# Kernel optimization log

Hardware: AMD Instinct MI355X
Metric: run time of the kernel (lower is better)

Reference implementation:

```python
import jax, jax.numpy as jnp
import numpy as np

N = 50000
E = 800000
IN_C = 128
HID = 64
HEADS = 4
NUM_CLASSES = 10
NUM_GRAPHS = 64
EPS = 1e-5
NEG_SLOPE = 0.2


def setup_inputs() -> dict:
    key = jax.random.key(0)
    ks = jax.random.split(key, 32)
    inp = {}
    inp["x"] = jax.random.normal(ks[0], (N, IN_C), dtype=jnp.float32)
    inp["edge_index"] = jax.random.randint(ks[1], (2, E), 0, N, dtype=jnp.int32)
    inp["batch"] = jnp.sort(jax.random.randint(ks[2], (N,), 0, NUM_GRAPHS, dtype=jnp.int32))
    s = 0.05
    # GATConv1: in=128 -> heads=4, hid=64, concat -> 256
    inp["W1"] = jax.random.normal(ks[3], (IN_C, HEADS * HID), dtype=jnp.float32) * s
    inp["a_src1"] = jax.random.normal(ks[4], (HEADS, HID), dtype=jnp.float32) * s
    inp["a_dst1"] = jax.random.normal(ks[5], (HEADS, HID), dtype=jnp.float32) * s
    inp["b1"] = jnp.zeros((HEADS * HID,), dtype=jnp.float32)
    inp["g1"] = jnp.ones((HEADS * HID,), dtype=jnp.float32)
    inp["be1"] = jnp.zeros((HEADS * HID,), dtype=jnp.float32)
    # GATConv2: in=256 -> heads=4, hid=64, concat -> 256
    inp["W2"] = jax.random.normal(ks[6], (HEADS * HID, HEADS * HID), dtype=jnp.float32) * s
    inp["a_src2"] = jax.random.normal(ks[7], (HEADS, HID), dtype=jnp.float32) * s
    inp["a_dst2"] = jax.random.normal(ks[8], (HEADS, HID), dtype=jnp.float32) * s
    inp["b2"] = jnp.zeros((HEADS * HID,), dtype=jnp.float32)
    inp["g2"] = jnp.ones((HEADS * HID,), dtype=jnp.float32)
    inp["be2"] = jnp.zeros((HEADS * HID,), dtype=jnp.float32)
    # GATConv3: in=256 -> heads=1, hid=64, mean (concat=False) -> 64
    inp["W3"] = jax.random.normal(ks[9], (HEADS * HID, 1 * HID), dtype=jnp.float32) * s
    inp["a_src3"] = jax.random.normal(ks[10], (1, HID), dtype=jnp.float32) * s
    inp["a_dst3"] = jax.random.normal(ks[11], (1, HID), dtype=jnp.float32) * s
    inp["b3"] = jnp.zeros((HID,), dtype=jnp.float32)
    inp["g3"] = jnp.ones((HID,), dtype=jnp.float32)
    inp["be3"] = jnp.zeros((HID,), dtype=jnp.float32)
    # final classifier
    inp["fcW"] = jax.random.normal(ks[12], (HID, NUM_CLASSES), dtype=jnp.float32) * s
    inp["fcb"] = jnp.zeros((NUM_CLASSES,), dtype=jnp.float32)
    return inp


def gat_conv(x, src, dst, W, a_src, a_dst, b, heads, out_c, concat):
    # Linear transform, split heads: [N, H, C]
    h = (x @ W).reshape(-1, heads, out_c)
    # Per-node attention logits (dot with per-head attention vectors): [N, H]
    as_ = jnp.einsum("nhc,hc->nh", h, a_src)
    ad_ = jnp.einsum("nhc,hc->nh", h, a_dst)
    # Per-edge unnormalized attention (src contributes a_src, dst a_dst)
    e = jax.nn.leaky_relu(as_[src] + ad_[dst], NEG_SLOPE)  # [E, H]
    # Segment softmax over destination node (stable)
    e_max = jax.ops.segment_max(e, dst, num_segments=N)  # [N, H]
    ex = jnp.exp(e - e_max[dst])
    denom = jax.ops.segment_sum(ex, dst, num_segments=N)  # [N, H]
    alpha = ex / denom[dst]  # [E, H]
    # Weighted scatter-aggregate of source features
    msg = h[src] * alpha[:, :, None]  # [E, H, C]
    out = jax.ops.segment_sum(msg, dst, num_segments=N)  # [N, H, C]
    out = out.reshape(-1, heads * out_c) if concat else out.mean(axis=1)
    return out + b


def batch_norm(x, gamma, beta):
    mean = x.mean(axis=0)
    var = x.var(axis=0)
    return (x - mean) * jax.lax.rsqrt(var + EPS) * gamma + beta


def reference(x, edge_index, batch, W1, a_src1, a_dst1, b1, g1, be1,
              W2, a_src2, a_dst2, b2, g2, be2,
              W3, a_src3, a_dst3, b3, g3, be3, fcW, fcb):
    src, dst = edge_index[0], edge_index[1]
    h = jax.nn.relu(gat_conv(x, src, dst, W1, a_src1, a_dst1, b1, HEADS, HID, True))
    h = batch_norm(h, g1, be1)  # dropout = identity (eval)
    h = jax.nn.relu(gat_conv(h, src, dst, W2, a_src2, a_dst2, b2, HEADS, HID, True))
    h = batch_norm(h, g2, be2)
    h = jax.nn.relu(gat_conv(h, src, dst, W3, a_src3, a_dst3, b3, 1, HID, False))
    h = batch_norm(h, g3, be3)
    # global mean pool over graphs
    sums = jax.ops.segment_sum(h, batch, num_segments=NUM_GRAPHS)  # [G, HID]
    counts = jax.ops.segment_sum(jnp.ones((h.shape[0],), h.dtype), batch, num_segments=NUM_GRAPHS)
    pooled = sums / jnp.maximum(counts, 1.0)[:, None]
    return pooled @ fcW + fcb
```

## Files before the change

kernel.cpp:

```cpp
#include <hip/hip_runtime.h>
#include <hip/hip_bf16.h>

#define N_NODES 50000
#define NUM_E   800000
#define EPS_BN  1e-5f
#define NUM_GRAPHS 64
#define NCOPY 64

typedef __attribute__((ext_vector_type(8))) short bf16x8;
typedef __attribute__((ext_vector_type(4))) float f32x4;
typedef unsigned short ushort_t;
typedef unsigned int uint_t;

static __device__ __forceinline__ unsigned short f2bf(float f) {
    unsigned int u = __float_as_uint(f);
    u += 0x7fffu + ((u >> 16) & 1u);
    return (unsigned short)(u >> 16);
}
static __device__ __forceinline__ uint_t pkbf(float lo, float hi) {
    __hip_bfloat162 t = __float22bfloat162_rn(make_float2(lo, hi));
    return *(uint_t*)&t;
}
static __device__ __forceinline__ float bflo(uint_t u) { return __uint_as_float(u << 16); }
static __device__ __forceinline__ float bfhi(uint_t u) { return __uint_as_float(u & 0xffff0000u); }

__global__ void hist_prep_kernel(const int* __restrict__ ei, int* __restrict__ deg,
                                 const float* __restrict__ W1, const float* __restrict__ W2,
                                 const float* __restrict__ W3, const float* __restrict__ x,
                                 ushort_t* __restrict__ w1t, ushort_t* __restrict__ w2t,
                                 ushort_t* __restrict__ w3t, ushort_t* __restrict__ xbf) {
    const int HB = (NUM_E + 255) / 256;
    const int S1 = 128 * 256, S2 = 256 * 256, S3 = 256 * 64;
    const int SW = S1 + S2 + S3;
    const int SX = N_NODES * 128 / 4;
    int b = blockIdx.x;
    if (b < HB) {
        int e = b * 256 + threadIdx.x;
        if (e < NUM_E) atomicAdd(&deg[ei[NUM_E + e]], 1);
        return;
    }
    int i = (b - HB) * 256 + threadIdx.x;
    if (i < SX) {
        float4 v = ((const float4*)x)[i];
        ((uint2*)xbf)[i] = make_uint2(pkbf(v.x, v.y), pkbf(v.z, v.w));
    } else if (i < SX + SW) {
        int j = i - SX;
        if (j < S1) {
            int k = j / 256, n = j % 256;
            w1t[n * 128 + k] = f2bf(W1[j]);
        } else if (j < S1 + S2) {
            int jj = j - S1; int k = jj / 256, n = jj % 256;
            w2t[n * 256 + k] = f2bf(W2[jj]);
        } else {
            int jj = j - S1 - S2; int k = jj / 64, n = jj % 64;
            w3t[n * 256 + k] = f2bf(W3[jj]);
        }
    }
}

__global__ void scan_local_kernel(const int* __restrict__ deg, int* __restrict__ rowptr,
                                  int* __restrict__ bsum) {
    __shared__ int ws[4];
    int b = blockIdx.x, t = threadIdx.x;
    int i = b * 256 + t;
    int lane = t & 63, wv = t >> 6;
    int v = (i < N_NODES) ? deg[i] : 0;
    int incl = v;
#pragma unroll
    for (int off = 1; off < 64; off <<= 1) {
        int u = __shfl_up(incl, off, 64);
        if (lane >= off) incl += u;
    }
    if (lane == 63) ws[wv] = incl;
    __syncthreads();
    if (t == 0) {
        int s = 0;
#pragma unroll
        for (int k = 0; k < 4; ++k) { int x = ws[k]; ws[k] = s; s += x; }
        bsum[b] = s;
    }
    __syncthreads();
    if (i < N_NODES) rowptr[i + 1] = ws[wv] + incl;
}

__global__ __launch_bounds__(256) void scan_fixup_kernel(int* __restrict__ rowptr,
                                                         const int* __restrict__ bsum) {
    __shared__ int ws[4];
    int b = blockIdx.x, t = threadIdx.x;
    int lane = t & 63, wv = t >> 6;
    int v = (t < b) ? bsum[t] : 0;
#pragma unroll
    for (int off = 1; off < 64; off <<= 1) v += __shfl_xor(v, off, 64);
    if (lane == 0) ws[wv] = v;
    __syncthreads();
    int pre = ws[0] + ws[1] + ws[2] + ws[3];
    int i = b * 256 + t;
    if (i < N_NODES) rowptr[i + 1] += pre;
    if (b == 0 && t == 0) rowptr[0] = 0;
}

template<int K, int NFULL, int BN, bool SCAT>
__global__ __launch_bounds__(256) void gemm_fused_kernel(const ushort_t* __restrict__ A,
                                                         const ushort_t* __restrict__ Bt,
                                                         ushort_t* __restrict__ C,
                                                         const float* __restrict__ stats,
                                                         const float* __restrict__ g,
                                                         const float* __restrict__ be,
                                                         const float* __restrict__ a_src,
                                                         const float* __restrict__ a_dst,
                                                         float* __restrict__ as_,
                                                         float* __restrict__ ad_,
                                                         const int* __restrict__ ei,
                                                         const int* __restrict__ rowptr,
                                                         int* __restrict__ fill,
                                                         int* __restrict__ srcs) {
    constexpr int GBX = (N_NODES + 127) / 128;
    if constexpr (SCAT) {
        if (blockIdx.x >= GBX) {
            int idx = (blockIdx.x - GBX) + 1563 * blockIdx.y;
            int e = idx * 256 + (int)threadIdx.x;
            if (e < NUM_E) {
                int dst = ei[NUM_E + e];
                int pos = rowptr[dst] + atomicAdd(&fill[dst], 1);
                srcs[pos] = ei[e];
            }
            return;
        }
    }
    const int NT = BN / 16;
    const int NG = BN / 64;
    constexpr int LOOP_BYTES = (128 * 40 + BN * 40) * 2;
    constexpr int EPI_BYTES  = 4 * 32 * 64 * 2;
    constexpr int SMEM_BYTES = LOOP_BYTES > EPI_BYTES ? LOOP_BYTES : EPI_BYTES;
    __shared__ __align__(16) unsigned char smem[SMEM_BYTES];
    ushort_t (*As)[40]     = (ushort_t (*)[40])smem;
    ushort_t (*Bs)[40]     = (ushort_t (*)[40])(smem + 128 * 40 * 2);
    ushort_t (*Cs)[32][64] = (ushort_t (*)[32][64])smem;
    __shared__ __align__(16) float aff_a[K], aff_b[K];
    __shared__ float asrc_s[BN], adst_s[BN];
    int tid = threadIdx.x;
    int lane = tid & 63, w = tid >> 6;
    int row0 = blockIdx.x * 128, col0 = blockIdx.y * BN;
    int m_l = lane & 15, q = lane >> 4;

    for (int c = tid; c < K; c += 256) {
        float a = 1.f, b = 0.f;
        if (stats) {
            float s0 = 0.f, s1 = 0.f;
#pragma unroll 8
            for (int j = 0; j < NCOPY; ++j) {
                s0 += stats[j * 512 + c];
                s1 += stats[j * 512 + 256 + c];
            }
            float m = s0 * (1.f / N_NODES);
            float var = fmaxf(s1 * (1.f / N_NODES) - m * m, 0.f);
            float rs = rsqrtf(var + EPS_BN) * g[c];
            a = rs; b = be[c] - m * rs;
        }
        aff_a[c] = a; aff_b[c] = b;
    }
    if (tid < BN) {
        asrc_s[tid] = a_src[col0 + tid];
        adst_s[tid] = a_dst[col0 + tid];
    }
    __syncthreads();

    f32x4 acc[2][NT];
#pragma unroll
    for (int r = 0; r < 2; ++r)
#pragma unroll
        for (int c = 0; c < NT; ++c) acc[r][c] = (f32x4){0.f, 0.f, 0.f, 0.f};

    int ar = tid >> 1, ako = (tid & 1) * 16;

    for (int k0 = 0; k0 < K; k0 += 32) {
        uint_t ow[8];
        int gr = row0 + ar;
        uint4 u0 = make_uint4(0, 0, 0, 0), u1 = make_uint4(0, 0, 0, 0);
        if (gr < N_NODES) {
            const ushort_t* ap = A + (long)gr * K + k0 + ako;
            u0 = *(const uint4*)ap;
            u1 = *(const uint4*)(ap + 8);
        }
        uint_t uu[8] = {u0.x, u0.y, u0.z, u0.w, u1.x, u1.y, u1.z, u1.w};
#pragma unroll
        for (int t = 0; t < 8; ++t) {
            int k = k0 + ako + t * 2;
            float lo = bflo(uu[t]) * aff_a[k] + aff_b[k];
            float hi = bfhi(uu[t]) * aff_a[k + 1] + aff_b[k + 1];
            ow[t] = pkbf(lo, hi);
        }
        if constexpr (BN == 128) {
            int br = tid >> 1, bko = (tid & 1) * 16;
            const ushort_t* bp = Bt + (long)(col0 + br) * K + k0 + bko;
            uint4 b0 = *(const uint4*)bp;
            uint4 b1 = *(const uint4*)(bp + 8);
            *(uint4*)&As[ar][ako] = make_uint4(ow[0], ow[1], ow[2], ow[3]);
            *(uint4*)&As[ar][ako + 8] = make_uint4(ow[4], ow[5], ow[6], ow[7]);
            *(uint4*)&Bs[br][bko] = b0;
            *(uint4*)&Bs[br][bko + 8] = b1;
        } else {
            int br = tid >> 2, bko = (tid & 3) * 8;
            uint4 bv = *(const uint4*)(Bt + (long)(col0 + br) * K + k0 + bko);
            *(uint4*)&As[ar][ako] = make_uint4(ow[0], ow[1], ow[2], ow[3]);
            *(uint4*)&As[ar][ako + 8] = make_uint4(ow[4], ow[5], ow[6], ow[7]);
            *(uint4*)&Bs[br][bko] = bv;
        }
        __syncthreads();

        bf16x8 af[2];
#pragma unroll
        for (int r = 0; r < 2; ++r)
            af[r] = *(const bf16x8*)&As[w * 32 + r * 16 + m_l][q * 8];
#pragma unroll
        for (int c = 0; c < NT; ++c) {
            bf16x8 bf = *(const bf16x8*)&Bs[c * 16 + m_l][q * 8];
#pragma unroll
            for (int r = 0; r < 2; ++r)
                acc[r][c] = __builtin_amdgcn_mfma_f32_16x16x32_bf16(af[r], bf, acc[r][c], 0, 0, 0);
        }
        __syncthreads();
    }

    const int H = NFULL / 64;
#pragma unroll
    for (int gblk = 0; gblk < NG; ++gblk) {
        int hidx = blockIdx.y * NG + gblk;
        int colg = col0 + gblk * 64;
#pragma unroll
        for (int r = 0; r < 2; ++r)
#pragma unroll
            for (int cc = 0; cc < 4; ++cc)
#pragma unroll
                for (int i = 0; i < 4; ++i)
                    Cs[w][r * 16 + q * 4 + i][cc * 16 + m_l] = f2bf(acc[r][gblk * 4 + cc][i]);
#pragma unroll
        for (int j = 0; j < 4; ++j) {
            int flat = j * 64 + lane;
            int lr = flat >> 3, chg = flat & 7;
            int gr = row0 + w * 32 + lr;
            uint4 u = *(uint4*)&Cs[w][lr][chg * 8];
            float f0 = bflo(u.x), f1 = bfhi(u.x), f2 = bflo(u.y), f3 = bfhi(u.y);
            float f4 = bflo(u.z), f5 = bfhi(u.z), f6 = bflo(u.w), f7 = bfhi(u.w);
            int cb = gblk * 64 + chg * 8;
            float s1 = f0 * asrc_s[cb] + f1 * asrc_s[cb + 1] + f2 * asrc_s[cb + 2] + f3 * asrc_s[cb + 3]
                     + f4 * asrc_s[cb + 4] + f5 * asrc_s[cb + 5] + f6 * asrc_s[cb + 6] + f7 * asrc_s[cb + 7];
            float s2 = f0 * adst_s[cb] + f1 * adst_s[cb + 1] + f2 * adst_s[cb + 2] + f3 * adst_s[cb + 3]
                     + f4 * adst_s[cb + 4] + f5 * adst_s[cb + 5] + f6 * adst_s[cb + 6] + f7 * adst_s[cb + 7];
#pragma unroll
            for (int o = 1; o < 8; o <<= 1) {
                s1 += __shfl_xor(s1, o, 64);
                s2 += __shfl_xor(s2, o, 64);
            }
            if (gr < N_NODES) {
                *(uint4*)(C + (long)gr * NFULL + colg + chg * 8) = u;
                if ((lane & 7) == 0) {
                    as_[gr * H + hidx] = s1;
                    ad_[gr * H + hidx] = s2;
                }
            }
        }
    }
}

__global__ __launch_bounds__(256) void agg4_kernel(const ushort_t* __restrict__ h,
                                                   const float* __restrict__ as_,
                                                   const float* __restrict__ ad_,
                                                   const int* __restrict__ rowptr,
                                                   const int* __restrict__ srcs,
                                                   const float* __restrict__ bias,
                                                   ushort_t* __restrict__ out) {
    __shared__ float4 alf[4][4][17];
    __shared__ int    sed[4][4][17];
    int tid = threadIdx.x;
    int lane = tid & 63, w = tid >> 6;
    int q = lane >> 4, cl = lane & 15;
    int n = blockIdx.x * 16 + w * 4 + q;

    int start = rowptr[n];
    int deg = rowptr[n + 1] - start;

    float4 adv = *(const float4*)(ad_ + n * 4);
    float ad4[4] = {adv.x, adv.y, adv.z, adv.w};

    float mx[4] = {-1e30f, -1e30f, -1e30f, -1e30f};
    float dn[4] = {0.f, 0.f, 0.f, 0.f};
    {
        float vst[4] = {-1e30f, -1e30f, -1e30f, -1e30f};
        int s0 = 0;
        if (deg > 0) s0 = srcs[start + min(cl, deg - 1)];
        sed[w][q][cl] = s0;
        if (cl < deg) {
            float4 av = *(const float4*)(as_ + s0 * 4);
            float vv[4] = {av.x + ad4[0], av.y + ad4[1], av.z + ad4[2], av.w + ad4[3]};
#pragma unroll
            for (int hh = 0; hh < 4; ++hh) {
                float v = vv[hh] > 0.f ? vv[hh] : 0.2f * vv[hh];
                vst[hh] = v; mx[hh] = v; dn[hh] = 1.f;
            }
        }
        alf[w][q][cl] = make_float4(vst[0], vst[1], vst[2], vst[3]);
        for (int j = cl + 16; j < deg; j += 16) {
            int s = srcs[start + j];
            float4 av = *(const float4*)(as_ + s * 4);
            float vv[4] = {av.x + ad4[0], av.y + ad4[1], av.z + ad4[2], av.w + ad4[3]};
#pragma unroll
            for (int hh = 0; hh < 4; ++hh) {
                float v = vv[hh] > 0.f ? vv[hh] : 0.2f * vv[hh];
                float mn = fmaxf(mx[hh], v);
                dn[hh] = dn[hh] * __expf(mx[hh] - mn) + __expf(v - mn);
                mx[hh] = mn;
            }
        }
    }
    float mloc[4] = {mx[0], mx[1], mx[2], mx[3]};
#pragma unroll
    for (int off = 1; off < 16; off <<= 1)
#pragma unroll
        for (int hh = 0; hh < 4; ++hh) mx[hh] = fmaxf(mx[hh], __shfl_xor(mx[hh], off, 64));
#pragma unroll
    for (int hh = 0; hh < 4; ++hh) dn[hh] *= __expf(mloc[hh] - mx[hh]);
#pragma unroll
    for (int off = 1; off < 16; off <<= 1)
#pragma unroll
        for (int hh = 0; hh < 4; ++hh) dn[hh] += __shfl_xor(dn[hh], off, 64);
    float inv[4];
#pragma unroll
    for (int hh = 0; hh < 4; ++hh) inv[hh] = dn[hh] > 0.f ? 1.f / dn[hh] : 0.f;
    {
        float4 vv = alf[w][q][cl];
        alf[w][q][cl] = make_float4(__expf(vv.x - mx[0]) * inv[0], __expf(vv.y - mx[1]) * inv[1],
                                    __expf(vv.z - mx[2]) * inv[2], __expf(vv.w - mx[3]) * inv[3]);
    }

    int hd = cl >> 2, cbase = cl * 16;
    float acc[16];
#pragma unroll
    for (int k = 0; k < 16; ++k) acc[k] = 0.f;

    for (int chunk = 0; chunk < deg || chunk == 0; chunk += 16) {
        if (chunk > 0) {
            int j = chunk + cl;
            int s = srcs[start + min(j, deg - 1)];
            sed[w][q][cl] = s;
            float a4[4] = {0.f, 0.f, 0.f, 0.f};
            if (j < deg) {
                float4 av = *(const float4*)(as_ + s * 4);
                float vv[4] = {av.x + ad4[0], av.y + ad4[1], av.z + ad4[2], av.w + ad4[3]};
#pragma unroll
                for (int hh = 0; hh < 4; ++hh) {
                    float v = vv[hh] > 0.f ? vv[hh] : 0.2f * vv[hh];
                    a4[hh] = __expf(v - mx[hh]) * inv[hh];
                }
            }
            alf[w][q][cl] = make_float4(a4[0], a4[1], a4[2], a4[3]);
        }
        int cnt = min(16, deg - chunk);
        if (cnt < 0) cnt = 0;
        int e = 0;
        for (; e + 4 <= cnt; e += 4) {
            float av[4]; int sv[4];
#pragma unroll
            for (int t = 0; t < 4; ++t) {
                av[t] = ((const float*)&alf[w][q][e + t])[hd];
                sv[t] = sed[w][q][e + t];
            }
            uint4 ua[4];
#pragma unroll
            for (int t = 0; t < 4; ++t)
                ua[t] = *(const uint4*)(h + (long)sv[t] * 256 + cbase);
#pragma unroll
            for (int t = 0; t < 4; ++t) {
                float al = av[t];
                acc[0] += al * bflo(ua[t].x); acc[1] += al * bfhi(ua[t].x);
                acc[2] += al * bflo(ua[t].y); acc[3] += al * bfhi(ua[t].y);
                acc[4] += al * bflo(ua[t].z); acc[5] += al * bfhi(ua[t].z);
                acc[6] += al * bflo(ua[t].w); acc[7] += al * bfhi(ua[t].w);
            }
#pragma unroll
            for (int t = 0; t < 4; ++t)
                ua[t] = *(const uint4*)(h + (long)sv[t] * 256 + cbase + 8);
#pragma unroll
            for (int t = 0; t < 4; ++t) {
                float al = av[t];
                acc[8]  += al * bflo(ua[t].x); acc[9]  += al * bfhi(ua[t].x);
                acc[10] += al * bflo(ua[t].y); acc[11] += al * bfhi(ua[t].y);
                acc[12] += al * bflo(ua[t].z); acc[13] += al * bfhi(ua[t].z);
                acc[14] += al * bflo(ua[t].w); acc[15] += al * bfhi(ua[t].w);
            }
        }
        for (; e < cnt; ++e) {
            float al = ((const float*)&alf[w][q][e])[hd];
            const ushort_t* hr = h + (long)sed[w][q][e] * 256 + cbase;
            uint4 u0 = *(const uint4*)hr;
            uint4 u1 = *(const uint4*)(hr + 8);
            acc[0]  += al * bflo(u0.x); acc[1]  += al * bfhi(u0.x);
            acc[2]  += al * bflo(u0.y); acc[3]  += al * bfhi(u0.y);
            acc[4]  += al * bflo(u0.z); acc[5]  += al * bfhi(u0.z);
            acc[6]  += al * bflo(u0.w); acc[7]  += al * bfhi(u0.w);
            acc[8]  += al * bflo(u1.x); acc[9]  += al * bfhi(u1.x);
            acc[10] += al * bflo(u1.y); acc[11] += al * bfhi(u1.y);
            acc[12] += al * bflo(u1.z); acc[13] += al * bfhi(u1.z);
            acc[14] += al * bflo(u1.w); acc[15] += al * bfhi(u1.w);
        }
        if (deg <= 16) break;
    }

    uint_t ow[8];
#pragma unroll
    for (int t = 0; t < 8; ++t) {
        float lo = fmaxf(acc[t * 2] + bias[cbase + t * 2], 0.f);
        float hi = fmaxf(acc[t * 2 + 1] + bias[cbase + t * 2 + 1], 0.f);
        ow[t] = pkbf(lo, hi);
    }
    ushort_t* op = out + (long)n * 256 + cbase;
    *(uint4*)op = make_uint4(ow[0], ow[1], ow[2], ow[3]);
    *(uint4*)(op + 8) = make_uint4(ow[4], ow[5], ow[6], ow[7]);
}

__global__ __launch_bounds__(256) void agg1_kernel(const ushort_t* __restrict__ h,
                                                   const float* __restrict__ as_,
                                                   const float* __restrict__ ad_,
                                                   const int* __restrict__ rowptr,
                                                   const int* __restrict__ srcs,
                                                   const float* __restrict__ bias,
                                                   ushort_t* __restrict__ out,
                                                   float* __restrict__ stats) {
    __shared__ float alf1[4][8][9];
    __shared__ int   sed1[4][8][9];
    __shared__ float ssum[64], ssq[64];
    int tid = threadIdx.x;
    int lane = tid & 63, w = tid >> 6;
    int o = lane >> 3, cl = lane & 7;
    int n = blockIdx.x * 32 + w * 8 + o;
    bool valid = n < N_NODES;
    int nc = valid ? n : N_NODES - 1;
    if (tid < 64) { ssum[tid] = 0.f; ssq[tid] = 0.f; }
    __syncthreads();

    int start = rowptr[nc];
    int deg = valid ? rowptr[nc + 1] - start : 0;
    float adn = ad_[nc];

    float mx = -1e30f, dn = 0.f;
    {
        float vst = -1e30f;
        int s0 = 0;
        if (deg > 0) s0 = srcs[start + min(cl, deg - 1)];
        sed1[w][o][cl] = s0;
        if (cl < deg) {
            float v = as_[s0] + adn;
            v = v > 0.f ? v : 0.2f * v;
            vst = v; mx = v; dn = 1.f;
        }
        alf1[w][o][cl] = vst;
        for (int j = cl + 8; j < deg; j += 8) {
            int s = srcs[start + j];
            float v = as_[s] + adn;
            v = v > 0.f ? v : 0.2f * v;
            float mn = fmaxf(mx, v);
            dn = dn * __expf(mx - mn) + __expf(v - mn);
            mx = mn;
        }
    }
    float mloc = mx;
#pragma unroll
    for (int off = 1; off < 8; off <<= 1) mx = fmaxf(mx, __shfl_xor(mx, off, 64));
    dn *= __expf(mloc - mx);
#pragma unroll
    for (int off = 1; off < 8; off <<= 1) dn += __shfl_xor(dn, off, 64);
    float inv = dn > 0.f ? 1.f / dn : 0.f;

    alf1[w][o][cl] = __expf(alf1[w][o][cl] - mx) * inv;

    int c0 = cl * 8;
    float acc[8] = {0.f, 0.f, 0.f, 0.f, 0.f, 0.f, 0.f, 0.f};

    for (int chunk = 0; chunk < deg || chunk == 0; chunk += 8) {
        if (chunk > 0) {
            int j = chunk + cl;
            int s = srcs[start + min(j, deg - 1)];
            sed1[w][o][cl] = s;
            float al = 0.f;
            if (j < deg) {
                float v = as_[s] + adn;
                v = v > 0.f ? v : 0.2f * v;
                al = __expf(v - mx) * inv;
            }
            alf1[w][o][cl] = al;
        }
        int cnt = min(8, deg - chunk);
        if (cnt < 0) cnt = 0;
        int e = 0;
        for (; e + 4 <= cnt; e += 4) {
            float av[4]; int sv[4];
#pragma unroll
            for (int t = 0; t < 4; ++t) {
                av[t] = alf1[w][o][e + t];
                sv[t] = sed1[w][o][e + t];
            }
            uint4 ua[4];
#pragma unroll
            for (int t = 0; t < 4; ++t)
                ua[t] = *(const uint4*)(h + (long)sv[t] * 64 + c0);
#pragma unroll
            for (int t = 0; t < 4; ++t) {
                float al = av[t];
                acc[0] += al * bflo(ua[t].x); acc[1] += al * bfhi(ua[t].x);
                acc[2] += al * bflo(ua[t].y); acc[3] += al * bfhi(ua[t].y);
                acc[4] += al * bflo(ua[t].z); acc[5] += al * bfhi(ua[t].z);
                acc[6] += al * bflo(ua[t].w); acc[7] += al * bfhi(ua[t].w);
            }
        }
        for (; e < cnt; ++e) {
            float al = alf1[w][o][e];
            uint4 u = *(const uint4*)(h + (long)sed1[w][o][e] * 64 + c0);
            acc[0] += al * bflo(u.x); acc[1] += al * bfhi(u.x);
            acc[2] += al * bflo(u.y); acc[3] += al * bfhi(u.y);
            acc[4] += al * bflo(u.z); acc[5] += al * bfhi(u.z);
            acc[6] += al * bflo(u.w); acc[7] += al * bfhi(u.w);
        }
        if (deg <= 8) break;
    }

    float v[8];
#pragma unroll
    for (int t = 0; t < 8; ++t) v[t] = fmaxf(acc[t] + bias[c0 + t], 0.f);
    if (valid) {
        uint_t ow[4];
#pragma unroll
        for (int t = 0; t < 4; ++t) ow[t] = pkbf(v[2 * t], v[2 * t + 1]);
        *(uint4*)(out + (long)n * 64 + c0) = make_uint4(ow[0], ow[1], ow[2], ow[3]);
    }
    float s1[8], s2[8];
#pragma unroll
    for (int t = 0; t < 8; ++t) {
        s1[t] = valid ? v[t] : 0.f;
        s2[t] = valid ? v[t] * v[t] : 0.f;
    }
#pragma unroll
    for (int off = 8; off < 64; off <<= 1)
#pragma unroll
        for (int t = 0; t < 8; ++t) {
            s1[t] += __shfl_xor(s1[t], off, 64);
            s2[t] += __shfl_xor(s2[t], off, 64);
        }
    if (lane < 8) {
#pragma unroll
        for (int t = 0; t < 8; ++t) {
            atomicAdd(&ssum[c0 + t], s1[t]);
            atomicAdd(&ssq[c0 + t], s2[t]);
        }
    }
    __syncthreads();
    if (tid < 64) {
        int cp = (blockIdx.x & (NCOPY - 1)) * 512;
        atomicAdd(&stats[cp + tid], ssum[tid]);
        atomicAdd(&stats[cp + 256 + tid], ssq[tid]);
    }
}

template<int C>
__global__ __launch_bounds__(256) void bn_stats_bf16(const ushort_t* __restrict__ x,
                                                     float* __restrict__ stats) {
    const int GROUPS = C / 8;
    const int RS = 256 / GROUPS;
    int tid = threadIdx.x;
    int cg_ = tid % GROUPS;
    int rs = tid / GROUPS;
    float s[8], s2[8];
#pragma unroll
    for (int k = 0; k < 8; ++k) { s[k] = 0.f; s2[k] = 0.f; }
    for (int n = blockIdx.x * RS + rs; n < N_NODES; n += gridDim.x * RS) {
        uint4 u = *(const uint4*)(x + (long)n * C + cg_ * 8);
        float f[8] = {bflo(u.x), bfhi(u.x), bflo(u.y), bfhi(u.y),
                      bflo(u.z), bfhi(u.z), bflo(u.w), bfhi(u.w)};
#pragma unroll
        for (int k = 0; k < 8; ++k) { s[k] += f[k]; s2[k] += f[k] * f[k]; }
    }
    __shared__ float red[256][16];
#pragma unroll
    for (int k = 0; k < 8; ++k) { red[tid][k] = s[k]; red[tid][8 + k] = s2[k]; }
    __syncthreads();
    if (tid < C) {
        int g = tid >> 3, k = tid & 7;
        float a = 0.f, b = 0.f;
        for (int r = 0; r < RS; ++r) {
            a += red[g + r * GROUPS][k];
            b += red[g + r * GROUPS][8 + k];
        }
        int cp = (blockIdx.x & (NCOPY - 1)) * 512;
        atomicAdd(&stats[cp + tid], a);
        atomicAdd(&stats[cp + 256 + tid], b);
    }
}

__global__ __launch_bounds__(256) void pool_fc_kernel(const ushort_t* __restrict__ h,
                                                      const int* __restrict__ batch,
                                                      const float* __restrict__ stats,
                                                      const float* __restrict__ g3,
                                                      const float* __restrict__ be3,
                                                      const float* __restrict__ fcW,
                                                      const float* __restrict__ fcb,
                                                      float* __restrict__ out) {
    int g = blockIdx.x;
    __shared__ int se[2];
    if (threadIdx.x < 2) {
        int gg = g + threadIdx.x;
        int lo = 0, hi = N_NODES;
        while (lo < hi) {
            int mid = (lo + hi) >> 1;
            if (batch[mid] < gg) lo = mid + 1; else hi = mid;
        }
        se[threadIdx.x] = lo;
    }
    __syncthreads();
    int s = se[0], e = se[1];
    int c = threadIdx.x & 63;
    int ty = threadIdx.x >> 6;
    float sum = 0.f;
    for (int n = s + ty; n < e; n += 4) sum += bflo((uint_t)h[(long)n * 64 + c]);
    __shared__ float red[4][64];
    __shared__ float pv[64];
    red[ty][c] = sum;
    __syncthreads();
    if (ty == 0) {
        float tot = red[0][c] + red[1][c] + red[2][c] + red[3][c];
        float v = tot / fmaxf((float)(e - s), 1.f);
        float s0 = 0.f, s1 = 0.f;
#pragma unroll 8
        for (int j = 0; j < NCOPY; ++j) {
            s0 += stats[j * 512 + c];
            s1 += stats[j * 512 + 256 + c];
        }
        float m = s0 * (1.f / N_NODES);
        float var = fmaxf(s1 * (1.f / N_NODES) - m * m, 0.f);
        pv[c] = (v - m) * rsqrtf(var + EPS_BN) * g3[c] + be3[c];
    }
    __syncthreads();
    if (threadIdx.x < 10) {
        int j = threadIdx.x;
        float acc = fcb[j];
#pragma unroll
        for (int k = 0; k < 64; ++k) acc += pv[k] * fcW[k * 10 + j];
        out[g * 10 + j] = acc;
    }
}

extern "C" void kernel_launch(void* const* d_in, const int* in_sizes, int n_in,
                              void* d_out, int out_size, void* d_ws, size_t ws_size,
                              hipStream_t stream) {
    const float* x      = (const float*)d_in[0];
    const int*   ei     = (const int*)d_in[1];
    const int*   batch  = (const int*)d_in[2];
    const float* W1     = (const float*)d_in[3];
    const float* a_src1 = (const float*)d_in[4];
    const float* a_dst1 = (const float*)d_in[5];
    const float* b1     = (const float*)d_in[6];
    const float* g1     = (const float*)d_in[7];
    const float* be1    = (const float*)d_in[8];
    const float* W2     = (const float*)d_in[9];
    const float* a_src2 = (const float*)d_in[10];
    const float* a_dst2 = (const float*)d_in[11];
    const float* b2     = (const float*)d_in[12];
    const float* g2     = (const float*)d_in[13];
    const float* be2    = (const float*)d_in[14];
    const float* W3     = (const float*)d_in[15];
    const float* a_src3 = (const float*)d_in[16];
    const float* a_dst3 = (const float*)d_in[17];
    const float* b3     = (const float*)d_in[18];
    const float* g3     = (const float*)d_in[19];
    const float* be3    = (const float*)d_in[20];
    const float* fcW    = (const float*)d_in[21];
    const float* fcb    = (const float*)d_in[22];
    float* out = (float*)d_out;

    const size_t N = N_NODES, E = NUM_E;
    const int SST = NCOPY * 512;
    ushort_t* hbf    = (ushort_t*)d_ws;
    ushort_t* hagg   = hbf + N * 256;
    ushort_t* xbf    = hagg + N * 256;
    ushort_t* w1t    = xbf + N * 128;
    ushort_t* w2t    = w1t + 256 * 128;
    ushort_t* w3t    = w2t + 256 * 256;
    float*    as_    = (float*)(w3t + 64 * 256 + 128);
    float*    ad_    = as_ + N * 4;
    int*      deg    = (int*)(ad_ + N * 4);
    int*      fill   = deg + N;
    float*    statsA = (float*)(fill + N);
    float*    statsB = statsA + SST;
    float*    statsC = statsB + SST;
    int*      rowptr = (int*)(statsC + SST);
    int*      srcs   = rowptr + (N + 1);
    int*      bsum   = srcs + E;

    const int NB = (N_NODES + 255) / 256;
    const int HB = (NUM_E + 255) / 256;
    const int SX = N_NODES * 128 / 4;
    const int SW = 128 * 256 + 256 * 256 + 256 * 64;
    const int PB = (SX + SW + 255) / 256;

    hipMemsetAsync(deg, 0, sizeof(int) * (2 * N + 3 * SST), stream);
    hist_prep_kernel<<<HB + PB, 256, 0, stream>>>(ei, deg, W1, W2, W3, x, w1t, w2t, w3t, xbf);
    scan_local_kernel<<<NB, 256, 0, stream>>>(deg, rowptr, bsum);
    scan_fixup_kernel<<<NB, 256, 0, stream>>>(rowptr, bsum);

    const int GB = (N_NODES + 127) / 128;
    const int AB = N_NODES / 16;

    gemm_fused_kernel<128, 256, 128, true><<<dim3(GB + 1563, 2), 256, 0, stream>>>(
        xbf, w1t, hbf, nullptr, nullptr, nullptr, a_src1, a_dst1, as_, ad_,
        ei, rowptr, fill, srcs);
    agg4_kernel<<<AB, 256, 0, stream>>>(hbf, as_, ad_, rowptr, srcs, b1, hagg);
    bn_stats_bf16<256><<<128, 256, 0, stream>>>(hagg, statsA);

    gemm_fused_kernel<256, 256, 128, false><<<dim3(GB, 2), 256, 0, stream>>>(
        hagg, w2t, hbf, statsA, g1, be1, a_src2, a_dst2, as_, ad_,
        nullptr, nullptr, nullptr, nullptr);
    agg4_kernel<<<AB, 256, 0, stream>>>(hbf, as_, ad_, rowptr, srcs, b2, hagg);
    bn_stats_bf16<256><<<128, 256, 0, stream>>>(hagg, statsB);

    gemm_fused_kernel<256, 64, 64, false><<<dim3(GB, 1), 256, 0, stream>>>(
        hagg, w3t, hbf, statsB, g2, be2, a_src3, a_dst3, as_, ad_,
        nullptr, nullptr, nullptr, nullptr);
    agg1_kernel<<<(N_NODES + 31) / 32, 256, 0, stream>>>(hbf, as_, ad_, rowptr, srcs, b3, hagg, statsC);

    pool_fc_kernel<<<NUM_GRAPHS, 256, 0, stream>>>(hagg, batch, statsC, g3, be3, fcW, fcb, out);
}
```

Before: 499.8 us.

## Fold batch-norm affine into GEMM weights and load tiles directly to LDS

Batch-norm scale is now folded into the next layer's weight matrix by a small new kernel, and the shift becomes a per-column bias vector added in the GEMM epilogue. This removes the per-element affine transform of the A operand inside the GEMM loop. That in turn lets the A and B tiles be loaded with global_load_lds straight into unpadded shared memory, skipping register staging. In exchange it adds two small kernel launches and the padded-row removal may raise LDS bank conflicts. Node buffers are padded so the unguarded row loads stay in bounds.

After: 480.2 us. 3.9% less time.

```diff
diff --git a/kernel.cpp b/kernel.cpp
--- a/kernel.cpp
+++ b/kernel.cpp
@@ -99,13 +99,40 @@
     if (b == 0 && t == 0) rowptr[0] = 0;
 }
 
+__global__ __launch_bounds__(256) void scale_w_kernel(const float* __restrict__ stats,
+                                                      const float* __restrict__ g,
+                                                      const float* __restrict__ be,
+                                                      const ushort_t* __restrict__ wt,
+                                                      ushort_t* __restrict__ wts,
+                                                      float* __restrict__ cvec) {
+    int n = blockIdx.x, k = threadIdx.x;
+    float s0 = 0.f, s1 = 0.f;
+#pragma unroll 8
+    for (int j = 0; j < NCOPY; ++j) {
+        s0 += stats[j * 512 + k];
+        s1 += stats[j * 512 + 256 + k];
+    }
+    float m = s0 * (1.f / N_NODES);
+    float var = fmaxf(s1 * (1.f / N_NODES) - m * m, 0.f);
+    float rs = rsqrtf(var + EPS_BN) * g[k];
+    float b = be[k] - m * rs;
+    float wv = bflo((uint_t)wt[n * 256 + k]);
+    wts[n * 256 + k] = f2bf(rs * wv);
+    float p = b * wv;
+    __shared__ float ws[4];
+    int lane = k & 63, wid = k >> 6;
+#pragma unroll
+    for (int off = 1; off < 64; off <<= 1) p += __shfl_xor(p, off, 64);
+    if (lane == 0) ws[wid] = p;
+    __syncthreads();
+    if (k == 0) cvec[n] = ws[0] + ws[1] + ws[2] + ws[3];
+}
+
 template<int K, int NFULL, int BN, bool SCAT>
 __global__ __launch_bounds__(256) void gemm_fused_kernel(const ushort_t* __restrict__ A,
                                                          const ushort_t* __restrict__ Bt,
                                                          ushort_t* __restrict__ C,
-                                                         const float* __restrict__ stats,
-                                                         const float* __restrict__ g,
-                                                         const float* __restrict__ be,
+                                                         const float* __restrict__ cvec,
                                                          const float* __restrict__ a_src,
                                                          const float* __restrict__ a_dst,
                                                          float* __restrict__ as_,
@@ -129,41 +156,25 @@
     }
     const int NT = BN / 16;
     const int NG = BN / 64;
-    constexpr int LOOP_BYTES = (128 * 40 + BN * 40) * 2;
+    constexpr int LOOP_BYTES = (128 * 32 + BN * 32) * 2;
     constexpr int EPI_BYTES  = 4 * 32 * 64 * 2;
     constexpr int SMEM_BYTES = LOOP_BYTES > EPI_BYTES ? LOOP_BYTES : EPI_BYTES;
     __shared__ __align__(16) unsigned char smem[SMEM_BYTES];
-    ushort_t (*As)[40]     = (ushort_t (*)[40])smem;
-    ushort_t (*Bs)[40]     = (ushort_t (*)[40])(smem + 128 * 40 * 2);
+    ushort_t* As = (ushort_t*)smem;
+    ushort_t* Bs = As + 128 * 32;
     ushort_t (*Cs)[32][64] = (ushort_t (*)[32][64])smem;
-    __shared__ __align__(16) float aff_a[K], aff_b[K];
+    __shared__ float cvec_s[BN];
     __shared__ float asrc_s[BN], adst_s[BN];
     int tid = threadIdx.x;
     int lane = tid & 63, w = tid >> 6;
     int row0 = blockIdx.x * 128, col0 = blockIdx.y * BN;
     int m_l = lane & 15, q = lane >> 4;
 
-    for (int c = tid; c < K; c += 256) {
-        float a = 1.f, b = 0.f;
-        if (stats) {
-            float s0 = 0.f, s1 = 0.f;
-#pragma unroll 8
-            for (int j = 0; j < NCOPY; ++j) {
-                s0 += stats[j * 512 + c];
-                s1 += stats[j * 512 + 256 + c];
-            }
-            float m = s0 * (1.f / N_NODES);
-            float var = fmaxf(s1 * (1.f / N_NODES) - m * m, 0.f);
-            float rs = rsqrtf(var + EPS_BN) * g[c];
-            a = rs; b = be[c] - m * rs;
-        }
-        aff_a[c] = a; aff_b[c] = b;
-    }
     if (tid < BN) {
+        cvec_s[tid] = cvec[col0 + tid];
         asrc_s[tid] = a_src[col0 + tid];
         adst_s[tid] = a_dst[col0 + tid];
     }
-    __syncthreads();
 
     f32x4 acc[2][NT];
 #pragma unroll
@@ -171,50 +182,32 @@
 #pragma unroll
         for (int c = 0; c < NT; ++c) acc[r][c] = (f32x4){0.f, 0.f, 0.f, 0.f};
 
-    int ar = tid >> 1, ako = (tid & 1) * 16;
+    int rsub = lane >> 2;
+    int csub = (lane & 3) * 8;
 
     for (int k0 = 0; k0 < K; k0 += 32) {
-        uint_t ow[8];
-        int gr = row0 + ar;
-        uint4 u0 = make_uint4(0, 0, 0, 0), u1 = make_uint4(0, 0, 0, 0);
-        if (gr < N_NODES) {
-            const ushort_t* ap = A + (long)gr * K + k0 + ako;
-            u0 = *(const uint4*)ap;
-            u1 = *(const uint4*)(ap + 8);
-        }
-        uint_t uu[8] = {u0.x, u0.y, u0.z, u0.w, u1.x, u1.y, u1.z, u1.w};
-#pragma unroll
-        for (int t = 0; t < 8; ++t) {
-            int k = k0 + ako + t * 2;
-            float lo = bflo(uu[t]) * aff_a[k] + aff_b[k];
-            float hi = bfhi(uu[t]) * aff_a[k + 1] + aff_b[k + 1];
-            ow[t] = pkbf(lo, hi);
+        {
+            const ushort_t* ag = A + (long)(row0 + w * 32 + rsub) * K + k0 + csub;
+            __builtin_amdgcn_global_load_lds(ag, As + (w * 32) * 32, 16, 0, 0);
+            __builtin_amdgcn_global_load_lds(ag + 16 * K, As + (w * 32 + 16) * 32, 16, 0, 0);
         }
         if constexpr (BN == 128) {
-            int br = tid >> 1, bko = (tid & 1) * 16;
-            const ushort_t* bp = Bt + (long)(col0 + br) * K + k0 + bko;
-            uint4 b0 = *(const uint4*)bp;
-            uint4 b1 = *(const uint4*)(bp + 8);
-            *(uint4*)&As[ar][ako] = make_uint4(ow[0], ow[1], ow[2], ow[3]);
-            *(uint4*)&As[ar][ako + 8] = make_uint4(ow[4], ow[5], ow[6], ow[7]);
-            *(uint4*)&Bs[br][bko] = b0;
-            *(uint4*)&Bs[br][bko + 8] = b1;
+            const ushort_t* bg = Bt + (long)(col0 + w * 32 + rsub) * K + k0 + csub;
+            __builtin_amdgcn_global_load_lds(bg, Bs + (w * 32) * 32, 16, 0, 0);
+            __builtin_amdgcn_global_load_lds(bg + 16 * K, Bs + (w * 32 + 16) * 32, 16, 0, 0);
         } else {
-            int br = tid >> 2, bko = (tid & 3) * 8;
-            uint4 bv = *(const uint4*)(Bt + (long)(col0 + br) * K + k0 + bko);
-            *(uint4*)&As[ar][ako] = make_uint4(ow[0], ow[1], ow[2], ow[3]);
-            *(uint4*)&As[ar][ako + 8] = make_uint4(ow[4], ow[5], ow[6], ow[7]);
-            *(uint4*)&Bs[br][bko] = bv;
+            const ushort_t* bg = Bt + (long)(col0 + w * 16 + rsub) * K + k0 + csub;
+            __builtin_amdgcn_global_load_lds(bg, Bs + (w * 16) * 32, 16, 0, 0);
         }
         __syncthreads();
 
         bf16x8 af[2];
 #pragma unroll
         for (int r = 0; r < 2; ++r)
-            af[r] = *(const bf16x8*)&As[w * 32 + r * 16 + m_l][q * 8];
+            af[r] = *(const bf16x8*)(As + (w * 32 + r * 16 + m_l) * 32 + q * 8);
 #pragma unroll
         for (int c = 0; c < NT; ++c) {
-            bf16x8 bf = *(const bf16x8*)&Bs[c * 16 + m_l][q * 8];
+            bf16x8 bf = *(const bf16x8*)(Bs + (c * 16 + m_l) * 32 + q * 8);
 #pragma unroll
             for (int r = 0; r < 2; ++r)
                 acc[r][c] = __builtin_amdgcn_mfma_f32_16x16x32_bf16(af[r], bf, acc[r][c], 0, 0, 0);
@@ -233,7 +226,8 @@
             for (int cc = 0; cc < 4; ++cc)
 #pragma unroll
                 for (int i = 0; i < 4; ++i)
-                    Cs[w][r * 16 + q * 4 + i][cc * 16 + m_l] = f2bf(acc[r][gblk * 4 + cc][i]);
+                    Cs[w][r * 16 + q * 4 + i][cc * 16 + m_l] =
+                        f2bf(acc[r][gblk * 4 + cc][i] + cvec_s[gblk * 64 + cc * 16 + m_l]);
 #pragma unroll
         for (int j = 0; j < 4; ++j) {
             int flat = j * 64 + lane;
@@ -676,23 +670,29 @@
     float* out = (float*)d_out;
 
     const size_t N = N_NODES, E = NUM_E;
+    const size_t NPAD = N + 128;
     const int SST = NCOPY * 512;
     ushort_t* hbf    = (ushort_t*)d_ws;
-    ushort_t* hagg   = hbf + N * 256;
-    ushort_t* xbf    = hagg + N * 256;
-    ushort_t* w1t    = xbf + N * 128;
+    ushort_t* hagg   = hbf + NPAD * 256;
+    ushort_t* xbf    = hagg + NPAD * 256;
+    ushort_t* w1t    = xbf + NPAD * 128;
     ushort_t* w2t    = w1t + 256 * 128;
     ushort_t* w3t    = w2t + 256 * 256;
-    float*    as_    = (float*)(w3t + 64 * 256 + 128);
+    ushort_t* w2ts   = w3t + 64 * 256;
+    ushort_t* w3ts   = w2ts + 256 * 256;
+    float*    as_    = (float*)(w3ts + 64 * 256 + 128);
     float*    ad_    = as_ + N * 4;
     int*      deg    = (int*)(ad_ + N * 4);
     int*      fill   = deg + N;
     float*    statsA = (float*)(fill + N);
     float*    statsB = statsA + SST;
     float*    statsC = statsB + SST;
-    int*      rowptr = (int*)(statsC + SST);
+    float*    cvec0  = statsC + SST;
+    int*      rowptr = (int*)(cvec0 + 256);
     int*      srcs   = rowptr + (N + 1);
     int*      bsum   = srcs + E;
+    float*    cvec2  = (float*)(bsum + 256);
+    float*    cvec3  = cvec2 + 256;
 
     const int NB = (N_NODES + 255) / 256;
     const int HB = (NUM_E + 255) / 256;
@@ -700,7 +700,7 @@
     const int SW = 128 * 256 + 256 * 256 + 256 * 64;
     const int PB = (SX + SW + 255) / 256;
 
-    hipMemsetAsync(deg, 0, sizeof(int) * (2 * N + 3 * SST), stream);
+    hipMemsetAsync(deg, 0, sizeof(int) * (2 * N + 3 * SST + 256), stream);
     hist_prep_kernel<<<HB + PB, 256, 0, stream>>>(ei, deg, W1, W2, W3, x, w1t, w2t, w3t, xbf);
     scan_local_kernel<<<NB, 256, 0, stream>>>(deg, rowptr, bsum);
     scan_fixup_kernel<<<NB, 256, 0, stream>>>(rowptr, bsum);
@@ -709,19 +709,21 @@
     const int AB = N_NODES / 16;
 
     gemm_fused_kernel<128, 256, 128, true><<<dim3(GB + 1563, 2), 256, 0, stream>>>(
-        xbf, w1t, hbf, nullptr, nullptr, nullptr, a_src1, a_dst1, as_, ad_,
+        xbf, w1t, hbf, cvec0, a_src1, a_dst1, as_, ad_,
         ei, rowptr, fill, srcs);
     agg4_kernel<<<AB, 256, 0, stream>>>(hbf, as_, ad_, rowptr, srcs, b1, hagg);
     bn_stats_bf16<256><<<128, 256, 0, stream>>>(hagg, statsA);
 
+    scale_w_kernel<<<256, 256, 0, stream>>>(statsA, g1, be1, w2t, w2ts, cvec2);
     gemm_fused_kernel<256, 256, 128, false><<<dim3(GB, 2), 256, 0, stream>>>(
-        hagg, w2t, hbf, statsA, g1, be1, a_src2, a_dst2, as_, ad_,
+        hagg, w2ts, hbf, cvec2, a_src2, a_dst2, as_, ad_,
         nullptr, nullptr, nullptr, nullptr);
     agg4_kernel<<<AB, 256, 0, stream>>>(hbf, as_, ad_, rowptr, srcs, b2, hagg);
     bn_stats_bf16<256><<<128, 256, 0, stream>>>(hagg, statsB);
 
+    scale_w_kernel<<<64, 256, 0, stream>>>(statsB, g2, be2, w3t, w3ts, cvec3);
     gemm_fused_kernel<256, 64, 64, false><<<dim3(GB, 1), 256, 0, stream>>>(
-        hagg, w3t, hbf, statsB, g2, be2, a_src3, a_dst3, as_, ad_,
+        hagg, w3ts, hbf, cvec3, a_src3, a_dst3, as_, ad_,
         nullptr, nullptr, nullptr, nullptr);
     agg1_kernel<<<(N_NODES + 31) / 32, 256, 0, stream>>>(hbf, as_, ad_, rowptr, srcs, b3, hagg, statsC);
 
```
